# Optimization experiments

Measured on AMD Instinct MI355X. Metric: run time of the kernel, lower is better.

Reference implementation:

```python
import jax, jax.numpy as jnp
import numpy as np
from jax.ops import segment_sum, segment_max

N = 50000        # nodes
E = 800000       # edges (before self loops)
IN_DIM = 128
HID = 16         # per-head out channels
HEADS = 4
NL = 3           # num GAT layers
OUT = 1
NG = 128         # number of graphs in the batch
NEG = 0.2        # LeakyReLU negative slope (PyG GATConv default)
EPS = 1e-5       # BatchNorm eps


def setup_inputs() -> dict:
    key = jax.random.key(0)
    ks = iter(jax.random.split(key, 64))
    inp = {}
    inp['x'] = jax.random.normal(next(ks), (N, IN_DIM), jnp.float32)
    inp['edge_index'] = jax.random.randint(next(ks), (2, E), 0, N, dtype=jnp.int32)
    inp['batch'] = jnp.sort(jax.random.randint(next(ks), (N,), 0, NG, dtype=jnp.int32))
    d = IN_DIM
    for l in range(NL):
        s = 1.0 / np.sqrt(d)
        inp[f'W{l}'] = jax.random.uniform(next(ks), (HEADS * HID, d), jnp.float32, -s, s)
        inp[f'att_src{l}'] = jax.random.normal(next(ks), (HEADS, HID), jnp.float32) * 0.1
        inp[f'att_dst{l}'] = jax.random.normal(next(ks), (HEADS, HID), jnp.float32) * 0.1
        inp[f'bias{l}'] = jnp.zeros((HEADS * HID,), jnp.float32)
        inp[f'gamma{l}'] = jnp.ones((HEADS * HID,), jnp.float32)
        inp[f'beta{l}'] = jnp.zeros((HEADS * HID,), jnp.float32)
        inp[f'mean{l}'] = jax.random.normal(next(ks), (HEADS * HID,), jnp.float32) * 0.1
        inp[f'var{l}'] = jax.random.uniform(next(ks), (HEADS * HID,), jnp.float32, 0.5, 1.5)
        d = HEADS * HID
    s = 1.0 / np.sqrt(d)
    inp['fcW'] = jax.random.uniform(next(ks), (OUT, d), jnp.float32, -s, s)
    inp['fcb'] = jnp.zeros((OUT,), jnp.float32)
    return inp


def gat_layer(x, src, dst, W, att_src, att_dst, bias):
    """PyG GATConv (concat=True). src/dst already include self loops."""
    n = x.shape[0]
    h = (x @ W.T).reshape(n, HEADS, HID)            # [N,H,C]
    a_s = jnp.sum(h * att_src, axis=-1)             # [N,H]
    a_d = jnp.sum(h * att_dst, axis=-1)             # [N,H]
    logits = a_s[src] + a_d[dst]                    # [Etot,H]
    logits = jnp.where(logits > 0, logits, NEG * logits)  # leaky_relu
    # scatter-softmax over destination-node neighborhoods
    m = segment_max(logits, dst, num_segments=n)
    e = jnp.exp(logits - m[dst])
    z = segment_sum(e, dst, num_segments=n)
    alpha = e / z[dst]                              # [Etot,H]
    out = segment_sum(h[src] * alpha[:, :, None], dst, num_segments=n)  # [N,H,C]
    return out.reshape(n, HEADS * HID) + bias, alpha


def reference(x, edge_index, batch,
              W0, att_src0, att_dst0, bias0, gamma0, beta0, mean0, var0,
              W1, att_src1, att_dst1, bias1, gamma1, beta1, mean1, var1,
              W2, att_src2, att_dst2, bias2, gamma2, beta2, mean2, var2,
              fcW, fcb):
    n = x.shape[0]
    loops = jnp.arange(n, dtype=edge_index.dtype)   # add_self_loops=True
    src = jnp.concatenate([edge_index[0], loops])
    dst = jnp.concatenate([edge_index[1], loops])
    params = [
        (W0, att_src0, att_dst0, bias0, gamma0, beta0, mean0, var0),
        (W1, att_src1, att_dst1, bias1, gamma1, beta1, mean1, var1),
        (W2, att_src2, att_dst2, bias2, gamma2, beta2, mean2, var2),
    ]
    h = x
    alpha0 = None
    for l, (W, a_s, a_d, b, g, be, mu, var) in enumerate(params):
        h, alpha = gat_layer(h, src, dst, W, a_s, a_d, b)
        if l == 0:
            alpha0 = alpha
        h = jax.nn.relu(h)
        h = g * (h - mu) / jnp.sqrt(var + EPS) + be  # BatchNorm1d (eval); dropout = identity
    # global_mean_pool over graph ids
    sums = segment_sum(h, batch, num_segments=NG)
    cnt = segment_sum(jnp.ones((n, 1), h.dtype), batch, num_segments=NG)
    pooled = sums / jnp.maximum(cnt, 1.0)
    out = jax.nn.sigmoid(pooled @ fcW.T + fcb)      # [NG, OUT]
    return out, alpha0
```

## Files before the change

kernel.cpp:

```cpp
#include <hip/hip_runtime.h>
#include <hip/hip_fp16.h>
#include <math.h>

#define NN     50000
#define EE     800000
#define ETOT   (EE + NN)
#define INDIM  128
#define HEADS  4
#define NG     128
#define NEGS   0.2f
#define BNEPS  1e-5f

typedef _Float16 half8 __attribute__((ext_vector_type(8)));
typedef _Float16 half4v __attribute__((ext_vector_type(4)));
typedef float floatx4 __attribute__((ext_vector_type(4)));


#define GEMMB  ((NN + 63) / 64)
#define HB     128
#define EPB    ((ETOT + HB - 1) / HB)
#define PASS2B ((NN + 255) / 256)

#define NX8    (NN * INDIM / 8)
#define PW1    (NX8 + 2048)
#define PW2    (PW1 + NG * 64)
#define PW3    (PW2 + NG)
#define PREPWB ((PW3 + 255) / 256)

__device__ __forceinline__ int edge_dst(const int* __restrict__ ei, int e) {
    return (e < EE) ? ei[EE + e] : (e - EE);
}
__device__ __forceinline__ int edge_src(const int* __restrict__ ei, int e) {
    return (e < EE) ? ei[e] : (e - EE);
}

__global__ __launch_bounds__(256) void prep_hist_kernel(
    const float* __restrict__ x, const float* __restrict__ W0,
    const float* __restrict__ W1, const float* __restrict__ W2,
    _Float16* __restrict__ Xh, _Float16* __restrict__ Wh,
    float* __restrict__ psums, int* __restrict__ pcnt,
    const int* __restrict__ ei, int* __restrict__ bh) {
    __shared__ int hist[256];
    int bid = blockIdx.x;
    int tid = threadIdx.x;
    if (bid < PREPWB) {
        int i = bid * 256 + tid;
        if (i < NX8) {
            float4 v0 = *(const float4*)(x + (size_t)i * 8);
            float4 v1 = *(const float4*)(x + (size_t)i * 8 + 4);
            half8 o;
            o[0] = (_Float16)v0.x; o[1] = (_Float16)v0.y;
            o[2] = (_Float16)v0.z; o[3] = (_Float16)v0.w;
            o[4] = (_Float16)v1.x; o[5] = (_Float16)v1.y;
            o[6] = (_Float16)v1.z; o[7] = (_Float16)v1.w;
            *(half8*)(Xh + (size_t)i * 8) = o;
        } else if (i < PW1) {
            int wi = (i - NX8) * 8;
#pragma unroll
            for (int j = 0; j < 8; ++j) {
                int idx = wi + j;
                float v = (idx < 8192) ? W0[idx]
                        : ((idx < 12288) ? W1[idx - 8192] : W2[idx - 12288]);
                Wh[idx] = (_Float16)v;
            }
        } else if (i < PW2) {
            psums[i - PW1] = 0.f;
        } else if (i < PW3) {
            pcnt[i - PW2] = 0;
        }
    } else {
        int hb = bid - PREPWB;
        hist[tid] = 0;
        __syncthreads();
        int base = hb * EPB;
        int end = min(base + EPB, ETOT);
        for (int e = base + tid; e < end; e += 256)
            atomicAdd(&hist[edge_dst(ei, e) >> 8], 1);
        __syncthreads();
        bh[tid * HB + hb] = hist[tid];
    }
}

__global__ __launch_bounds__(1024) void scan1_kernel(int* __restrict__ bh,
                                                     int* __restrict__ rowstart) {
    __shared__ int wsum[16];
    __shared__ int carryS;
    int tid = threadIdx.x;
    int lane = tid & 63;
    int w = tid >> 6;
    if (tid == 0) carryS = 0;
    __syncthreads();
    for (int c = 0; c < 32; ++c) {
        int idx = c * 1024 + tid;
        int v = bh[idx];
        int x = v;
#pragma unroll
        for (int off = 1; off < 64; off <<= 1) {
            int t = __shfl_up(x, off, 64);
            if (lane >= off) x += t;
        }
        if (lane == 63) wsum[w] = x;
        __syncthreads();
        if (w == 0 && lane < 16) {
            int s = wsum[lane];
#pragma unroll
            for (int off = 1; off < 16; off <<= 1) {
                int t = __shfl_up(s, off, 16);
                if ((lane & 15) >= off) s += t;
            }
            wsum[lane] = s;
        }
        __syncthreads();
        int incl = ((w > 0) ? wsum[w - 1] : 0) + x;
        int c0 = carryS;
        bh[idx] = c0 + incl - v;
        __syncthreads();
        if (tid == 1023) carryS = c0 + incl;
        __syncthreads();
    }
    if (tid == 0) rowstart[NN] = ETOT;
}

template <int DD>
__device__ __forceinline__ void gemm_att_body(
    int bid, const _Float16* __restrict__ X, const _Float16* __restrict__ Wh,
    const float* __restrict__ attS, const float* __restrict__ attD,
    _Float16* __restrict__ H, float* __restrict__ AS, float* __restrict__ ADZ) {
    constexpr int KB = DD / 32;
    int tid = threadIdx.x;
    int wv = tid >> 6;
    int lane = tid & 63;
    int quad = lane >> 4;
    int n = lane & 15;
    int wbase = bid * 64 + wv * 16;

    int arow = wbase + n;
    if (arow >= NN) arow = NN - 1;
    half8 a[KB];
#pragma unroll
    for (int kb = 0; kb < KB; ++kb)
        a[kb] = *(const half8*)(X + (size_t)arow * DD + kb * 32 + quad * 8);

    floatx4 c[4];
#pragma unroll
    for (int t = 0; t < 4; ++t) {
        floatx4 acc = {0.f, 0.f, 0.f, 0.f};
#pragma unroll
        for (int kb = 0; kb < KB; ++kb) {
            half8 b = *(const half8*)(Wh + (size_t)(t * 16 + n) * DD + kb * 32 + quad * 8);
            acc = __builtin_amdgcn_mfma_f32_16x16x32_f16(a[kb], b, acc, 0, 0, 0);
        }
        c[t] = acc;
    }

    float as_l[4], ad_l[4];
#pragma unroll
    for (int t = 0; t < 4; ++t) {
        as_l[t] = attS[t * 16 + n];
        ad_l[t] = attD[t * 16 + n];
    }
#pragma unroll
    for (int r = 0; r < 4; ++r) {
        int node = wbase + quad * 4 + r;
        bool ok = node < NN;
#pragma unroll
        for (int t = 0; t < 4; ++t) {
            float h = c[t][r];
            if (ok) H[(size_t)node * 64 + t * 16 + n] = (_Float16)h;
            float vs = h * as_l[t];
            float vd = h * ad_l[t];
#pragma unroll
            for (int off = 8; off; off >>= 1) {
                vs += __shfl_down(vs, off, 16);
                vd += __shfl_down(vd, off, 16);
            }
            if (ok && n == 0) {
                AS[node * 4 + t] = vs;
                ADZ[(size_t)node * 8 + t] = vd;
            }
        }
    }
}

__global__ __launch_bounds__(256) void gemm0_scatter1_kernel(
    const _Float16* __restrict__ X, const _Float16* __restrict__ Wh,
    const float* __restrict__ attS, const float* __restrict__ attD,
    _Float16* __restrict__ H, float* __restrict__ AS, float* __restrict__ ADZ,
    const int* __restrict__ ei, const int* __restrict__ bh,
    int2* __restrict__ tmp) {
    __shared__ int offs[256];
    if (blockIdx.x < GEMMB) {
        gemm_att_body<128>(blockIdx.x, X, Wh, attS, attD, H, AS, ADZ);
    } else {
        int sb = blockIdx.x - GEMMB;
        int tid = threadIdx.x;
        offs[tid] = bh[tid * HB + sb];
        __syncthreads();
        int base = sb * EPB;
        int end = min(base + EPB, ETOT);
        for (int e = base + tid; e < end; e += 256) {
            int d = edge_dst(ei, e);
            int s = edge_src(ei, e);
            int pos = atomicAdd(&offs[d >> 8], 1);
            int2 p; p.x = d; p.y = s;
            tmp[pos] = p;
        }
    }
}

__global__ __launch_bounds__(256) void pass2_kernel(
    const int2* __restrict__ tmp, const int* __restrict__ bh,
    int* __restrict__ csr, int* __restrict__ rowstart) {
    __shared__ int h2[256];
    __shared__ int offs[256];
    __shared__ int ws[4];
    int b = blockIdx.x;
    int tid = threadIdx.x;
    int lane = tid & 63;
    int w = tid >> 6;
    int A = bh[b * HB];
    int Bend = bh[(b + 1) * HB];
    h2[tid] = 0;
    __syncthreads();
    for (int idx = A + tid; idx < Bend; idx += 256)
        atomicAdd(&h2[tmp[idx].x & 255], 1);
    __syncthreads();
    int v = h2[tid];
    int x = v;
#pragma unroll
    for (int off = 1; off < 64; off <<= 1) {
        int t = __shfl_up(x, off, 64);
        if (lane >= off) x += t;
    }
    if (lane == 63) ws[w] = x;
    __syncthreads();
    if (tid == 0) {
        int s = 0;
#pragma unroll
        for (int j = 0; j < 4; ++j) { int t = ws[j]; ws[j] = s; s += t; }
    }
    __syncthreads();
    int ex = x - v + ws[w];
    int abs0 = A + ex;
    offs[tid] = abs0;
    int d = b * 256 + tid;
    if (d < NN) rowstart[d] = abs0;
    __syncthreads();
    for (int idx = A + tid; idx < Bend; idx += 256) {
        int2 p = tmp[idx];
        int pos = atomicAdd(&offs[p.x & 255], 1);
        csr[pos] = p.y;
    }
}

__device__ __forceinline__ void alpha_body(
    int bid, const int* __restrict__ ei, const float* __restrict__ AS,
    const float* __restrict__ ADZ, float* __restrict__ alpha_out) {
    int e = bid * 256 + threadIdx.x;
    if (e >= ETOT) return;
    int s = edge_src(ei, e);
    int d = edge_dst(ei, e);
    float4 as = *(const float4*)(AS + (size_t)s * 4);
    const float* row = ADZ + (size_t)d * 8;
    float4 ad = *(const float4*)(row);
    float4 z4 = *(const float4*)(row + 4);
    float l;
    float4 a;
    l = as.x + ad.x; l = l > 0.f ? l : NEGS * l; a.x = __expf(l) / z4.x;
    l = as.y + ad.y; l = l > 0.f ? l : NEGS * l; a.y = __expf(l) / z4.y;
    l = as.z + ad.z; l = l > 0.f ? l : NEGS * l; a.z = __expf(l) / z4.z;
    l = as.w + ad.w; l = l > 0.f ? l : NEGS * l; a.w = __expf(l) / z4.w;
    *(float4*)(alpha_out + (size_t)e * 4) = a;
}

#define SCATB  ((ETOT + 255) / 256)

__global__ __launch_bounds__(256) void gemm1_alpha_kernel(
    const _Float16* __restrict__ X, const _Float16* __restrict__ Wh,
    const float* __restrict__ attS, const float* __restrict__ attD,
    _Float16* __restrict__ H, float* __restrict__ ASb, float* __restrict__ ADZb,
    const int* __restrict__ ei, const float* __restrict__ ASa,
    const float* __restrict__ ADZa, float* __restrict__ alpha_out) {
    if (blockIdx.x < GEMMB)
        gemm_att_body<64>(blockIdx.x, X, Wh, attS, attD, H, ASb, ADZb);
    else
        alpha_body(blockIdx.x - GEMMB, ei, ASa, ADZa, alpha_out);
}

__global__ __launch_bounds__(256) void gemm2_kernel(
    const _Float16* __restrict__ X, const _Float16* __restrict__ Wh,
    const float* __restrict__ attS, const float* __restrict__ attD,
    _Float16* __restrict__ H, float* __restrict__ AS, float* __restrict__ ADZ) {
    gemm_att_body<64>(blockIdx.x, X, Wh, attS, attD, H, AS, ADZ);
}

template <bool WRITE_Z>
__global__ __launch_bounds__(256) void edge_aggr_kernel(
    const _Float16* __restrict__ H, const float* __restrict__ AS,
    float* __restrict__ ADZ,
    const int* __restrict__ rowstart,
    const int* __restrict__ csr,
    const float* __restrict__ bias, const float* __restrict__ gamma,
    const float* __restrict__ beta, const float* __restrict__ mean,
    const float* __restrict__ var, _Float16* __restrict__ Hout) {
    int v = (blockIdx.x * blockDim.x + threadIdx.x) >> 6;
    if (v >= NN) return;
    int lane = threadIdx.x & 63;
    int q = lane >> 4;
    int l16 = lane & 15;
    int head = l16 >> 2;
    int ch4 = l16 * 4;
    float adv = ADZ[(size_t)v * 8 + head];
    int start = rowstart[v];
    int cnt = rowstart[v + 1] - start;
    const int* srow = csr + start;
    int cm1 = cnt - 1;
    float z = 0.f;
    float acc0 = 0.f, acc1 = 0.f, acc2 = 0.f, acc3 = 0.f;
    for (int k = 0; k < cnt; k += 16) {
        int b = k + q * 4;
        int s0 = srow[min(b + 0, cm1)];
        int s1 = srow[min(b + 1, cm1)];
        int s2 = srow[min(b + 2, cm1)];
        int s3 = srow[min(b + 3, cm1)];
        float a0 = AS[(size_t)s0 * 4 + head];
        float a1 = AS[(size_t)s1 * 4 + head];
        float a2 = AS[(size_t)s2 * 4 + head];
        float a3 = AS[(size_t)s3 * 4 + head];
        half4v h0 = *(const half4v*)(H + (size_t)s0 * 64 + ch4);
        half4v h1 = *(const half4v*)(H + (size_t)s1 * 64 + ch4);
        half4v h2 = *(const half4v*)(H + (size_t)s2 * 64 + ch4);
        half4v h3 = *(const half4v*)(H + (size_t)s3 * 64 + ch4);
        float l0 = a0 + adv; l0 = l0 > 0.f ? l0 : NEGS * l0;
        float l1 = a1 + adv; l1 = l1 > 0.f ? l1 : NEGS * l1;
        float l2 = a2 + adv; l2 = l2 > 0.f ? l2 : NEGS * l2;
        float l3 = a3 + adv; l3 = l3 > 0.f ? l3 : NEGS * l3;
        float p0 = (b + 0 < cnt) ? __expf(l0) : 0.f;
        float p1 = (b + 1 < cnt) ? __expf(l1) : 0.f;
        float p2 = (b + 2 < cnt) ? __expf(l2) : 0.f;
        float p3 = (b + 3 < cnt) ? __expf(l3) : 0.f;
        z += (p0 + p1) + (p2 + p3);
        acc0 = fmaf(p0, (float)h0[0], acc0); acc1 = fmaf(p0, (float)h0[1], acc1);
        acc2 = fmaf(p0, (float)h0[2], acc2); acc3 = fmaf(p0, (float)h0[3], acc3);
        acc0 = fmaf(p1, (float)h1[0], acc0); acc1 = fmaf(p1, (float)h1[1], acc1);
        acc2 = fmaf(p1, (float)h1[2], acc2); acc3 = fmaf(p1, (float)h1[3], acc3);
        acc0 = fmaf(p2, (float)h2[0], acc0); acc1 = fmaf(p2, (float)h2[1], acc1);
        acc2 = fmaf(p2, (float)h2[2], acc2); acc3 = fmaf(p2, (float)h2[3], acc3);
        acc0 = fmaf(p3, (float)h3[0], acc0); acc1 = fmaf(p3, (float)h3[1], acc1);
        acc2 = fmaf(p3, (float)h3[2], acc2); acc3 = fmaf(p3, (float)h3[3], acc3);
    }
    z    += __shfl_xor(z, 16);    z    += __shfl_xor(z, 32);
    acc0 += __shfl_xor(acc0, 16); acc0 += __shfl_xor(acc0, 32);
    acc1 += __shfl_xor(acc1, 16); acc1 += __shfl_xor(acc1, 32);
    acc2 += __shfl_xor(acc2, 16); acc2 += __shfl_xor(acc2, 32);
    acc3 += __shfl_xor(acc3, 16); acc3 += __shfl_xor(acc3, 32);
    if (q == 0) {
        if (WRITE_Z && (l16 & 3) == 0) ADZ[(size_t)v * 8 + 4 + head] = z;
        float4 bi = *(const float4*)(bias + ch4);
        float4 ga = *(const float4*)(gamma + ch4);
        float4 be = *(const float4*)(beta + ch4);
        float4 mu = *(const float4*)(mean + ch4);
        float4 va = *(const float4*)(var + ch4);
        float r0 = fmaxf(acc0 / z + bi.x, 0.f);
        float r1 = fmaxf(acc1 / z + bi.y, 0.f);
        float r2 = fmaxf(acc2 / z + bi.z, 0.f);
        float r3 = fmaxf(acc3 / z + bi.w, 0.f);
        r0 = ga.x * (r0 - mu.x) * rsqrtf(va.x + BNEPS) + be.x;
        r1 = ga.y * (r1 - mu.y) * rsqrtf(va.y + BNEPS) + be.y;
        r2 = ga.z * (r2 - mu.z) * rsqrtf(va.z + BNEPS) + be.z;
        r3 = ga.w * (r3 - mu.w) * rsqrtf(va.w + BNEPS) + be.w;
        half4v o;
        o[0] = (_Float16)r0;
        o[1] = (_Float16)r1;
        o[2] = (_Float16)r2;
        o[3] = (_Float16)r3;
        *(half4v*)(Hout + (size_t)v * 64 + ch4) = o;
    }
}

__global__ __launch_bounds__(256) void pool_kernel(const __half* __restrict__ H,
                                                   const int* __restrict__ batch,
                                                   float* __restrict__ sums,
                                                   int* __restrict__ cnt) {
    int wid = (blockIdx.x * blockDim.x + threadIdx.x) >> 6;
    int lane = threadIdx.x & 63;
    int base = wid * 16;
    if (base >= NN) return;
    int end = min(base + 16, NN);
    int cur = batch[base];
    float acc = 0.f;
    int c0 = 0;
    for (int i = base; i < end; ++i) {
        int g = batch[i];
        if (g != cur) {
            atomicAdd(&sums[cur * 64 + lane], acc);
            if (lane == 0) atomicAdd(&cnt[cur], c0);
            cur = g; acc = 0.f; c0 = 0;
        }
        acc += __half2float(H[(size_t)i * 64 + lane]);
        c0++;
    }
    atomicAdd(&sums[cur * 64 + lane], acc);
    if (lane == 0) atomicAdd(&cnt[cur], c0);
}

__global__ void fc_kernel(const float* __restrict__ sums, const int* __restrict__ cnt,
                          const float* __restrict__ fcW, const float* __restrict__ fcb,
                          float* __restrict__ out) {
    int g = (blockIdx.x * blockDim.x + threadIdx.x) >> 6;
    int lane = threadIdx.x & 63;
    if (g >= NG) return;
    float c = fmaxf((float)cnt[g], 1.f);
    float val = (sums[g * 64 + lane] / c) * fcW[lane];
#pragma unroll
    for (int off = 32; off; off >>= 1) val += __shfl_down(val, off, 64);
    if (lane == 0) out[g] = 1.f / (1.f + expf(-(val + fcb[0])));
}

extern "C" void kernel_launch(void* const* d_in, const int* in_sizes, int n_in,
                              void* d_out, int out_size, void* d_ws, size_t ws_size,
                              hipStream_t stream) {
    const float* x   = (const float*)d_in[0];
    const int* ei    = (const int*)d_in[1];
    const int* batch = (const int*)d_in[2];
    const float* W[3], *attS[3], *attD[3], *bias[3], *gamma[3], *beta[3], *mean[3], *var[3];
    for (int l = 0; l < 3; ++l) {
        W[l]     = (const float*)d_in[3 + 8 * l + 0];
        attS[l]  = (const float*)d_in[3 + 8 * l + 1];
        attD[l]  = (const float*)d_in[3 + 8 * l + 2];
        bias[l]  = (const float*)d_in[3 + 8 * l + 3];
        gamma[l] = (const float*)d_in[3 + 8 * l + 4];
        beta[l]  = (const float*)d_in[3 + 8 * l + 5];
        mean[l]  = (const float*)d_in[3 + 8 * l + 6];
        var[l]   = (const float*)d_in[3 + 8 * l + 7];
    }
    const float* fcW = (const float*)d_in[27];
    const float* fcb = (const float*)d_in[28];
    float* out = (float*)d_out;
    float* alpha_out = (float*)d_out + NG;

    char* p = (char*)d_ws;
    auto carve = [&](size_t bytes) {
        char* q = p;
        p += (bytes + 255) & ~(size_t)255;
        return q;
    };
    _Float16* Xh    = (_Float16*)carve(sizeof(_Float16) * NN * INDIM);
    _Float16* Wh    = (_Float16*)carve(sizeof(_Float16) * 16384);
    _Float16* Hh    = (_Float16*)carve(sizeof(_Float16) * NN * 64);
    _Float16* Hn    = (_Float16*)carve(sizeof(_Float16) * NN * 64);
    float* ASa      = (float*)carve(sizeof(float) * NN * 4);
    float* ADZa     = (float*)carve(sizeof(float) * NN * 8);
    float* ASb      = (float*)carve(sizeof(float) * NN * 4);
    float* ADZb     = (float*)carve(sizeof(float) * NN * 8);
    int*   rowstart = (int*)carve(sizeof(int) * (NN + 1));
    int*   bh       = (int*)carve(sizeof(int) * 256 * HB);
    int2*  tmp      = (int2*)carve(sizeof(int2) * ETOT);
    int*   csr      = (int*)carve(sizeof(int) * ETOT);
    float* psums    = (float*)carve(sizeof(float) * NG * 64);
    int*   pcnt     = (int*)carve(sizeof(int) * NG);

    int edgeBlocks = (NN * 64 + 255) / 256;

    prep_hist_kernel<<<PREPWB + HB, 256, 0, stream>>>(
        x, W[0], W[1], W[2], Xh, Wh, psums, pcnt, ei, bh);

    scan1_kernel<<<1, 1024, 0, stream>>>(bh, rowstart);

    gemm0_scatter1_kernel<<<GEMMB + HB, 256, 0, stream>>>(
        Xh, Wh, attS[0], attD[0], Hh, ASa, ADZa, ei, bh, tmp);

    pass2_kernel<<<PASS2B, 256, 0, stream>>>(tmp, bh, csr, rowstart);

    edge_aggr_kernel<true><<<edgeBlocks, 256, 0, stream>>>(
        Hh, ASa, ADZa, rowstart, csr,
        bias[0], gamma[0], beta[0], mean[0], var[0], Hn);

    gemm1_alpha_kernel<<<GEMMB + SCATB, 256, 0, stream>>>(
        Hn, Wh + 8192, attS[1], attD[1], Hh, ASb, ADZb,
        ei, ASa, ADZa, alpha_out);

    edge_aggr_kernel<false><<<edgeBlocks, 256, 0, stream>>>(
        Hh, ASb, ADZb, rowstart, csr,
        bias[1], gamma[1], beta[1], mean[1], var[1], Hn);

    gemm2_kernel<<<GEMMB, 256, 0, stream>>>(
        Hn, Wh + 12288, attS[2], attD[2], Hh, ASa, ADZa);

    edge_aggr_kernel<false><<<edgeBlocks, 256, 0, stream>>>(
        Hh, ASa, ADZa, rowstart, csr,
        bias[2], gamma[2], beta[2], mean[2], var[2], Hn);

    int poolWaves = (NN + 15) / 16;
    pool_kernel<<<(poolWaves * 64 + 255) / 256, 256, 0, stream>>>(
        (const __half*)Hn, batch, psums, pcnt);

    fc_kernel<<<(NG * 64 + 255) / 256, 256, 0, stream>>>(psums, pcnt, fcW, fcb, out);
}
```

Baseline: 341.0 us.

## Pack CSR scatter entries, transpose bucket histogram, and stage pass2 segments in LDS

```diff
diff --git a/kernel.cpp b/kernel.cpp
--- a/kernel.cpp
+++ b/kernel.cpp
@@ -20,6 +20,7 @@
 #define HB     128
 #define EPB    ((ETOT + HB - 1) / HB)
 #define PASS2B ((NN + 255) / 256)
+#define SEGCAP 6144
 
 #define NX8    (NN * INDIM / 8)
 #define PW1    (NX8 + 2048)
@@ -77,48 +78,41 @@
         for (int e = base + tid; e < end; e += 256)
             atomicAdd(&hist[edge_dst(ei, e) >> 8], 1);
         __syncthreads();
-        bh[tid * HB + hb] = hist[tid];
-    }
-}
-
-__global__ __launch_bounds__(1024) void scan1_kernel(int* __restrict__ bh,
-                                                     int* __restrict__ rowstart) {
-    __shared__ int wsum[16];
-    __shared__ int carryS;
-    int tid = threadIdx.x;
-    int lane = tid & 63;
-    int w = tid >> 6;
-    if (tid == 0) carryS = 0;
-    __syncthreads();
-    for (int c = 0; c < 32; ++c) {
-        int idx = c * 1024 + tid;
-        int v = bh[idx];
-        int x = v;
-#pragma unroll
-        for (int off = 1; off < 64; off <<= 1) {
-            int t = __shfl_up(x, off, 64);
-            if (lane >= off) x += t;
-        }
-        if (lane == 63) wsum[w] = x;
-        __syncthreads();
-        if (w == 0 && lane < 16) {
-            int s = wsum[lane];
-#pragma unroll
-            for (int off = 1; off < 16; off <<= 1) {
-                int t = __shfl_up(s, off, 16);
-                if ((lane & 15) >= off) s += t;
-            }
-            wsum[lane] = s;
-        }
-        __syncthreads();
-        int incl = ((w > 0) ? wsum[w - 1] : 0) + x;
-        int c0 = carryS;
-        bh[idx] = c0 + incl - v;
-        __syncthreads();
-        if (tid == 1023) carryS = c0 + incl;
-        __syncthreads();
-    }
-    if (tid == 0) rowstart[NN] = ETOT;
+        bh[hb * 256 + tid] = hist[tid];
+    }
+}
+
+__global__ __launch_bounds__(256) void scan1_kernel(int* __restrict__ bh,
+                                                    int* __restrict__ rowstart) {
+    __shared__ int ws[4];
+    int t = threadIdx.x;
+    int lane = t & 63;
+    int w = t >> 6;
+    int sum = 0;
+#pragma unroll 8
+    for (int b = 0; b < HB; ++b) sum += bh[b * 256 + t];
+    int x = sum;
+#pragma unroll
+    for (int off = 1; off < 64; off <<= 1) {
+        int tt = __shfl_up(x, off, 64);
+        if (lane >= off) x += tt;
+    }
+    if (lane == 63) ws[w] = x;
+    __syncthreads();
+    if (t == 0) {
+        int s = 0;
+#pragma unroll
+        for (int j = 0; j < 4; ++j) { int tt = ws[j]; ws[j] = s; s += tt; }
+    }
+    __syncthreads();
+    int base = x - sum + ws[w];
+#pragma unroll 8
+    for (int b = 0; b < HB; ++b) {
+        int v = bh[b * 256 + t];
+        bh[b * 256 + t] = base;
+        base += v;
+    }
+    if (t == 0) rowstart[NN] = ETOT;
 }
 
 template <int DD>
@@ -187,14 +181,14 @@
     const float* __restrict__ attS, const float* __restrict__ attD,
     _Float16* __restrict__ H, float* __restrict__ AS, float* __restrict__ ADZ,
     const int* __restrict__ ei, const int* __restrict__ bh,
-    int2* __restrict__ tmp) {
+    int* __restrict__ tmp) {
     __shared__ int offs[256];
     if (blockIdx.x < GEMMB) {
         gemm_att_body<128>(blockIdx.x, X, Wh, attS, attD, H, AS, ADZ);
     } else {
         int sb = blockIdx.x - GEMMB;
         int tid = threadIdx.x;
-        offs[tid] = bh[tid * HB + sb];
+        offs[tid] = bh[sb * 256 + tid];
         __syncthreads();
         int base = sb * EPB;
         int end = min(base + EPB, ETOT);
@@ -202,54 +196,75 @@
             int d = edge_dst(ei, e);
             int s = edge_src(ei, e);
             int pos = atomicAdd(&offs[d >> 8], 1);
-            int2 p; p.x = d; p.y = s;
-            tmp[pos] = p;
-        }
-    }
-}
-
-__global__ __launch_bounds__(256) void pass2_kernel(
-    const int2* __restrict__ tmp, const int* __restrict__ bh,
+            tmp[pos] = s | ((d & 255) << 16);
+        }
+    }
+}
+
+__global__ __launch_bounds__(512) void pass2_kernel(
+    const int* __restrict__ tmp, const int* __restrict__ bh,
     int* __restrict__ csr, int* __restrict__ rowstart) {
+    __shared__ int pk[SEGCAP];
+    __shared__ int outv[SEGCAP];
     __shared__ int h2[256];
     __shared__ int offs[256];
     __shared__ int ws[4];
     int b = blockIdx.x;
     int tid = threadIdx.x;
-    int lane = tid & 63;
-    int w = tid >> 6;
-    int A = bh[b * HB];
-    int Bend = bh[(b + 1) * HB];
-    h2[tid] = 0;
-    __syncthreads();
-    for (int idx = A + tid; idx < Bend; idx += 256)
-        atomicAdd(&h2[tmp[idx].x & 255], 1);
-    __syncthreads();
-    int v = h2[tid];
-    int x = v;
-#pragma unroll
-    for (int off = 1; off < 64; off <<= 1) {
-        int t = __shfl_up(x, off, 64);
-        if (lane >= off) x += t;
-    }
-    if (lane == 63) ws[w] = x;
+    int A = bh[b];
+    int Bend = bh[b + 1];
+    int n = Bend - A;
+    bool fits = (n <= SEGCAP);
+    if (tid < 256) h2[tid] = 0;
+    __syncthreads();
+    if (fits) {
+        for (int i = tid; i < n; i += 512) pk[i] = tmp[A + i];
+        __syncthreads();
+        for (int i = tid; i < n; i += 512) atomicAdd(&h2[pk[i] >> 16], 1);
+    } else {
+        for (int i = tid; i < n; i += 512) atomicAdd(&h2[tmp[A + i] >> 16], 1);
+    }
+    __syncthreads();
+    int v = 0, x = 0;
+    if (tid < 256) {
+        int lane = tid & 63;
+        v = h2[tid];
+        x = v;
+#pragma unroll
+        for (int off = 1; off < 64; off <<= 1) {
+            int t2 = __shfl_up(x, off, 64);
+            if (lane >= off) x += t2;
+        }
+        if (lane == 63) ws[tid >> 6] = x;
+    }
     __syncthreads();
     if (tid == 0) {
         int s = 0;
 #pragma unroll
-        for (int j = 0; j < 4; ++j) { int t = ws[j]; ws[j] = s; s += t; }
-    }
-    __syncthreads();
-    int ex = x - v + ws[w];
-    int abs0 = A + ex;
-    offs[tid] = abs0;
-    int d = b * 256 + tid;
-    if (d < NN) rowstart[d] = abs0;
-    __syncthreads();
-    for (int idx = A + tid; idx < Bend; idx += 256) {
-        int2 p = tmp[idx];
-        int pos = atomicAdd(&offs[p.x & 255], 1);
-        csr[pos] = p.y;
+        for (int j = 0; j < 4; ++j) { int t2 = ws[j]; ws[j] = s; s += t2; }
+    }
+    __syncthreads();
+    if (tid < 256) {
+        int ex = x - v + ws[tid >> 6];
+        offs[tid] = ex;
+        int d = b * 256 + tid;
+        if (d < NN) rowstart[d] = A + ex;
+    }
+    __syncthreads();
+    if (fits) {
+        for (int i = tid; i < n; i += 512) {
+            int p = pk[i];
+            int pos = atomicAdd(&offs[p >> 16], 1);
+            outv[pos] = p & 0xFFFF;
+        }
+        __syncthreads();
+        for (int i = tid; i < n; i += 512) csr[A + i] = outv[i];
+    } else {
+        for (int i = tid; i < n; i += 512) {
+            int p = tmp[A + i];
+            int pos = atomicAdd(&offs[p >> 16], 1);
+            csr[A + pos] = p & 0xFFFF;
+        }
     }
 }
 
@@ -455,7 +470,7 @@
     float* ADZb     = (float*)carve(sizeof(float) * NN * 8);
     int*   rowstart = (int*)carve(sizeof(int) * (NN + 1));
     int*   bh       = (int*)carve(sizeof(int) * 256 * HB);
-    int2*  tmp      = (int2*)carve(sizeof(int2) * ETOT);
+    int*   tmp      = (int*)carve(sizeof(int) * ETOT);
     int*   csr      = (int*)carve(sizeof(int) * ETOT);
     float* psums    = (float*)carve(sizeof(float) * NG * 64);
     int*   pcnt     = (int*)carve(sizeof(int) * NG);
@@ -465,12 +480,12 @@
     prep_hist_kernel<<<PREPWB + HB, 256, 0, stream>>>(
         x, W[0], W[1], W[2], Xh, Wh, psums, pcnt, ei, bh);
 
-    scan1_kernel<<<1, 1024, 0, stream>>>(bh, rowstart);
+    scan1_kernel<<<1, 256, 0, stream>>>(bh, rowstart);
 
     gemm0_scatter1_kernel<<<GEMMB + HB, 256, 0, stream>>>(
         Xh, Wh, attS[0], attD[0], Hh, ASa, ADZa, ei, bh, tmp);
 
-    pass2_kernel<<<PASS2B, 256, 0, stream>>>(tmp, bh, csr, rowstart);
+    pass2_kernel<<<PASS2B, 512, 0, stream>>>(tmp, bh, csr, rowstart);
 
     edge_aggr_kernel<true><<<edgeBlocks, 256, 0, stream>>>(
         Hh, ASa, ADZa, rowstart, csr,
```

Result: faster. 312.8 us (median of 2 runs) (-8.3%).
